# Kernel tuning notes

Hardware: AMD Instinct MI355X
Metric: run time of the kernel (lower is better)

Reference implementation:

```python
import jax, jax.numpy as jnp
import numpy as np

# ---- static config (matches init_kwargs) ----
B, CIN, COUT, L = 8, 64, 64, 32768
K, STRIDE, PAD, DIL = 5, 1, 2, 1
G, DG = 4, 2                      # groups, deformable_groups_per_groups
GDG = G * DG
CD = CIN // GDG                   # channels per deformable group
DW = 7                            # depthwise kernel size of offset/mask branch
OFFSET_SCALE = 4.0
EPS = 1e-5
LOUT = (L + 2 * PAD - DIL * (K - 1) - 1) // STRIDE + 1


def setup_inputs() -> dict:
    key = jax.random.key(0)
    ks = jax.random.split(key, 8)
    s = 0.02
    f32 = jnp.float32
    return {
        "x": jax.random.normal(ks[0], (B, CIN, L), f32),
        # offset branch: depthwise conv -> per-channel groupnorm -> 1x1 conv
        "dw_off_w": (jax.random.normal(ks[1], (CIN, 1, DW), f32) * s),
        "dw_off_b": jnp.zeros((CIN,), f32),
        "gn_off_w": jnp.ones((CIN,), f32),
        "gn_off_b": jnp.zeros((CIN,), f32),
        "pw_off_w": (jax.random.normal(ks[2], (GDG * K, CIN), f32) * s),
        "pw_off_b": jnp.zeros((GDG * K,), f32),
        # attn-mask branch (same structure); final bias init to ones per repo
        "dw_m_w": (jax.random.normal(ks[3], (CIN, 1, DW), f32) * s),
        "dw_m_b": jnp.zeros((CIN,), f32),
        "gn_m_w": jnp.ones((CIN,), f32),
        "gn_m_b": jnp.zeros((CIN,), f32),
        "pw_m_w": (jax.random.normal(ks[4], (GDG * K, CIN), f32) * s),
        "pw_m_b": jnp.ones((GDG * K,), f32),
        # main conv weight (Cout, Cin/G, K) and bias, normal(0, 0.02)
        "weight": (jax.random.normal(ks[5], (COUT, CIN // G, K), f32) * s),
        "bias": (jax.random.normal(ks[6], (COUT,), f32) * s),
    }


def _dwconv(x, w, b):
    # depthwise conv1d, padding (DW-1)//2, groups = CIN
    y = jax.lax.conv_general_dilated(
        x, w, window_strides=(1,), padding=[((DW - 1) // 2, (DW - 1) // 2)],
        feature_group_count=CIN, dimension_numbers=("NCH", "OIH", "NCH"))
    return y + b[None, :, None]


def _gn_per_channel(x, g, b):
    # GroupNorm with num_groups == num_channels: normalize each channel over L
    mu = jnp.mean(x, axis=-1, keepdims=True)
    var = jnp.var(x, axis=-1, keepdims=True)
    return (x - mu) * jax.lax.rsqrt(var + EPS) * g[None, :, None] + b[None, :, None]


def _branch(x, dw_w, dw_b, gn_g, gn_b, pw_w, pw_b):
    h = _gn_per_channel(_dwconv(x, dw_w, dw_b), gn_g, gn_b)
    return jnp.einsum("oc,bcl->bol", pw_w, h) + pw_b[None, :, None]


def _deform_conv1d(x, offset, attn, weight, bias):
    # x: (B,CIN,L); offset/attn: (B,GDG*K,LOUT)
    xg = x.reshape(B, G, DG, CD, L)
    off = offset.reshape(B, G, DG, K, LOUT)
    # base sampling grid: l*stride - pad + k*dil   -> (K, LOUT)
    base = (jnp.arange(LOUT) * STRIDE - PAD)[None, :] + (jnp.arange(K) * DIL)[:, None]
    p = base.astype(x.dtype)[None, None, None] + off          # (B,G,DG,K,LOUT)
    p0 = jnp.floor(p)
    w1 = p - p0                                               # linear-interp weight
    p0i = p0.astype(jnp.int32)

    def gather(idx):
        valid = ((idx >= 0) & (idx < L)).astype(x.dtype)
        idxc = jnp.clip(idx, 0, L - 1).reshape(B, G, DG, 1, K * LOUT)
        idxc = jnp.broadcast_to(idxc, (B, G, DG, CD, K * LOUT))
        v = jnp.take_along_axis(xg, idxc, axis=-1).reshape(B, G, DG, CD, K, LOUT)
        return v * valid[:, :, :, None]

    sampled = gather(p0i) * (1.0 - w1)[:, :, :, None] + gather(p0i + 1) * w1[:, :, :, None]
    sampled = sampled * attn.reshape(B, G, DG, 1, K, LOUT)
    wg = weight.reshape(G, COUT // G, DG, CD, K)
    out = jnp.einsum("godck,bgdckl->bgol", wg, sampled).reshape(B, COUT, LOUT)
    return out + bias[None, :, None]


def reference(x, dw_off_w, dw_off_b, gn_off_w, gn_off_b, pw_off_w, pw_off_b,
              dw_m_w, dw_m_b, gn_m_w, gn_m_b, pw_m_w, pw_m_b, weight, bias):
    offset = _branch(x, dw_off_w, dw_off_b, gn_off_w, gn_off_b, pw_off_w, pw_off_b) * OFFSET_SCALE
    attn = _branch(x, dw_m_w, dw_m_b, gn_m_w, gn_m_b, pw_m_w, pw_m_b)
    # softmax modulation over the K kernel taps within each deformable group
    attn = jax.nn.softmax(attn.reshape(B, GDG, K, LOUT), axis=2).reshape(B, GDG * K, LOUT)
    return _deform_conv1d(x, offset, attn, weight, bias)
```

## Files before the change

### kernel.cpp

```cpp
#include <hip/hip_runtime.h>
#include <hip/hip_bf16.h>
#include <hip/hip_fp16.h>

typedef unsigned int   uint;
typedef unsigned short ushort;

#define NB   8
#define NC   64
#define LL   32768
#define KK   5
#define NG   4
#define NDG  2
#define NGD  8
#define NCD  8
#define NOFF 40
#define DWK  7
#define XROW (LL + 16)

typedef _Float16 f16x8 __attribute__((ext_vector_type(8)));
typedef float    f32x4 __attribute__((ext_vector_type(4)));

__device__ __forceinline__ uint pkrtz(float a, float b) {
  typedef __fp16 fp16x2n __attribute__((ext_vector_type(2)));
  fp16x2n h = __builtin_amdgcn_cvt_pkrtz(a, b);
  union { fp16x2n h; uint u; } v; v.h = h; return v.u;
}

__global__ __launch_bounds__(256) void k_prep(
    const float* __restrict__ pwA, const float* __restrict__ pwM,
    const float* __restrict__ mw,
    float* __restrict__ wtA, float* __restrict__ wtM, ushort* __restrict__ Wf)
{
  int idx = blockIdx.x * 256 + threadIdx.x;
  if (idx < 2560) {
    int c = idx / 40, o = idx % 40;
    wtA[idx] = pwA[o * NC + c];
  } else if (idx < 5120) {
    int j = idx - 2560;
    int c = j / 40, o = j % 40;
    wtM[j] = pwM[o * NC + c];
  } else if (idx < 11264) {
    int j  = idx - 5120;
    int jj = j & 7;
    int l  = (j >> 3) & 63;
    int gt = j >> 9;
    int t  = gt % 3, g = gt / 3;
    int o  = l & 15;
    int kq = t * 32 + ((l >> 4) << 3) + jj;
    float val = 0.f;
    if (kq < 80) {
      int ktap = kq >> 3, c = kq & 7;
      int d = ktap / 5, kh = ktap % 5;
      val = mw[((g * 16 + o) * 16 + d * 8 + c) * KK + kh];
    }
    Wf[j] = __half_as_ushort(__float2half(val));
  }
}

__device__ __forceinline__ void load8f(float* dst, const float* __restrict__ row,
                                       int start)
{
  if (start >= 0 && start + 8 <= LL) {
    float4 a = *(const float4*)(row + start);
    float4 b = *(const float4*)(row + start + 4);
    dst[0] = a.x; dst[1] = a.y; dst[2] = a.z; dst[3] = a.w;
    dst[4] = b.x; dst[5] = b.y; dst[6] = b.z; dst[7] = b.w;
  } else {
#pragma unroll
    for (int j = 0; j < 8; ++j) {
      int p = start + j;
      dst[j] = (p >= 0 && p < LL) ? row[p] : 0.f;
    }
  }
}

__global__ __launch_bounds__(256) void k_stat(
    const float* __restrict__ x,
    const float* __restrict__ dwAw, const float* __restrict__ dwAb,
    const float* __restrict__ dwMw, const float* __restrict__ dwMb,
    ushort* __restrict__ xT, float4* __restrict__ partial)
{
  __shared__ __align__(16) ushort lx[8 * 256];
  int tid  = threadIdx.x;
  int lblk = blockIdx.x & 127;
  int gd   = (blockIdx.x >> 7) & 7;
  int b    = blockIdx.x >> 10;
  int c    = tid >> 5;
  int q    = tid & 31;
  int l0   = lblk << 8;
  int lb   = l0 + q * 8;
  int ch   = gd * 8 + c;
  const float* row = x + (size_t)(b * NC + ch) * LL;

  float v[24];
  load8f(v + 0,  row, lb - 8);
  load8f(v + 8,  row, lb);
  load8f(v + 16, row, lb + 8);

  {
    uint4 xr;
    xr.x = pkrtz(v[8],  v[9]);
    xr.y = pkrtz(v[10], v[11]);
    xr.z = pkrtz(v[12], v[13]);
    xr.w = pkrtz(v[14], v[15]);
    *(uint4*)(lx + c * 256 + q * 8) = xr;
  }

  float wa[DWK], wm[DWK];
#pragma unroll
  for (int j = 0; j < DWK; ++j) {
    wa[j] = dwAw[ch * DWK + j];
    wm[j] = dwMw[ch * DWK + j];
  }
  float ba = dwAb[ch], bm = dwMb[ch];

  float sa = 0.f, qa = 0.f, sm = 0.f, qm = 0.f;
#pragma unroll
  for (int u = 0; u < 8; ++u) {
    float ya = ba, ym = bm;
#pragma unroll
    for (int j = 0; j < DWK; ++j) {
      float xv = v[5 + u + j];
      ya += wa[j] * xv;
      ym += wm[j] * xv;
    }
    sa += ya; qa += ya * ya;
    sm += ym; qm += ym * ym;
  }

#pragma unroll
  for (int m = 1; m < 32; m <<= 1) {
    sa += __shfl_xor(sa, m);
    qa += __shfl_xor(qa, m);
    sm += __shfl_xor(sm, m);
    qm += __shfl_xor(qm, m);
  }
  if (q == 0)
    partial[((size_t)(b * NC + ch) << 7) + lblk] = make_float4(sa, qa, sm, qm);

  __syncthreads();
  {
    uint4 pk;
    pk.x = (uint)lx[0 * 256 + tid] | ((uint)lx[1 * 256 + tid] << 16);
    pk.y = (uint)lx[2 * 256 + tid] | ((uint)lx[3 * 256 + tid] << 16);
    pk.z = (uint)lx[4 * 256 + tid] | ((uint)lx[5 * 256 + tid] << 16);
    pk.w = (uint)lx[6 * 256 + tid] | ((uint)lx[7 * 256 + tid] << 16);
    size_t rowbase = (size_t)(b * NGD + gd) * (size_t)XROW;
    *(uint4*)(xT + (rowbase + 8 + (size_t)(l0 + tid)) * 8) = pk;
    if (tid < 8) {
      uint4 z = {0, 0, 0, 0};
      if (lblk == 0)   *(uint4*)(xT + (rowbase + tid) * 8) = z;
      if (lblk == 127) *(uint4*)(xT + (rowbase + 8 + LL + tid) * 8) = z;
    }
  }
}

__global__ __launch_bounds__(256) void k_fin(
    const float4* __restrict__ partial,
    const float* __restrict__ gnAw, const float* __restrict__ gnAb,
    const float* __restrict__ gnMw, const float* __restrict__ gnMb,
    const float* __restrict__ wtA, const float* __restrict__ wtM,
    const float* __restrict__ pbA, const float* __restrict__ pbM,
    ushort* __restrict__ wFp, float* __restrict__ biasPt)
{
  __shared__ float4 pr[256];
  __shared__ float gA[64], cA[64], gM[64], cM[64];
  __shared__ float sbA[40], sbM[40];
  int b = blockIdx.x;
  int t = threadIdx.x;
  {
    int c = t & 63, seg = t >> 6;
    const float4* pp = partial + ((size_t)(b * NC + c) << 7);
    float4 s = make_float4(0.f, 0.f, 0.f, 0.f);
    for (int i = seg; i < 128; i += 4) {
      float4 u = pp[i];
      s.x += u.x; s.y += u.y; s.z += u.z; s.w += u.w;
    }
    pr[t] = s;
  }
  __syncthreads();
  if (t < 64) {
    float4 a0 = pr[t], a1 = pr[t + 64], a2 = pr[t + 128], a3 = pr[t + 192];
    float sx = a0.x + a1.x + a2.x + a3.x;
    float sy = a0.y + a1.y + a2.y + a3.y;
    float sz = a0.z + a1.z + a2.z + a3.z;
    float sw = a0.w + a1.w + a2.w + a3.w;
    float mua = sx / LL, vara = sy / LL - mua * mua;
    float mum = sz / LL, varm = sw / LL - mum * mum;
    float ga = gnAw[t] * rsqrtf(vara + 1e-5f);
    float gm = gnMw[t] * rsqrtf(varm + 1e-5f);
    gA[t] = ga; cA[t] = gnAb[t] - mua * ga;
    gM[t] = gm; cM[t] = gnMb[t] - mum * gm;
  }
  __syncthreads();
  if (t < 40) {
    float sA = 0.f, sM = 0.f;
    for (int c = 0; c < 64; ++c) {
      sA += wtA[c * 40 + t] * cA[c];
      sM += wtM[c * 40 + t] * cM[c];
    }
    sbA[t] = 4.f * (pbA[t] + sA);
    sbM[t] = pbM[t] + sM;
  }
  for (int idx = t; idx < 8192; idx += 256) {
    int br = idx >> 12;
    int e  = idx & 4095;
    int g  = e >> 10;
    int ks = (e >> 9) & 1;
    int ln = (e >> 3) & 63;
    int j  = e & 7;
    int rr = ln & 15;
    int c  = ks * 32 + ((ln >> 4) << 3) + j;
    float v = 0.f;
    if (rr < 10) {
      int o = 10 * g + rr;
      v = br ? wtM[c * 40 + o] * gM[c] : 4.f * wtA[c * 40 + o] * gA[c];
    }
    wFp[(size_t)b * 8192 + idx] = __half_as_ushort(__float2half(v));
  }
  __syncthreads();
  if (t < 128) {
    int br = t >> 6, g = (t >> 4) & 3, m = t & 15;
    float v = 0.f;
    if (m < 10) v = br ? sbM[10 * g + m] : sbA[10 * g + m];
    biasPt[b * 128 + t] = v;
  }
}

__global__ __launch_bounds__(256) void k_pd(
    const float* __restrict__ x,
    const float* __restrict__ dwAw, const float* __restrict__ dwAb,
    const float* __restrict__ dwMw, const float* __restrict__ dwMb,
    const ushort* __restrict__ xT,
    const ushort* __restrict__ wFp, const float* __restrict__ biasPt,
    const ushort* __restrict__ Wf, const float* __restrict__ bias,
    float* __restrict__ out)
{
  __shared__ __align__(16) char S[4 * 12288];
  int tid = threadIdx.x;
  int w   = tid >> 6;
  int ln  = tid & 63;
  int h   = ln >> 4;
  int col = ln & 15;
  int b   = blockIdx.x >> 9;
  int lb0 = (blockIdx.x & 511) << 6;

  {
    int cc = tid >> 2;
    int q  = tid & 3;
    int p0 = lb0 + q * 16;
    const float* row = x + (size_t)(b * NC + cc) * LL;
    float v[32];
    load8f(v + 0,  row, p0 - 8);
    load8f(v + 8,  row, p0);
    load8f(v + 16, row, p0 + 8);
    load8f(v + 24, row, p0 + 16);
    float wa[DWK], wm[DWK];
#pragma unroll
    for (int j = 0; j < DWK; ++j) {
      wa[j] = dwAw[cc * DWK + j];
      wm[j] = dwMw[cc * DWK + j];
    }
    float ba = dwAb[cc], bm = dwMb[cc];
    uint wbuf[16];
#pragma unroll
    for (int u = 0; u < 16; ++u) {
      float ya = ba, ym = bm;
#pragma unroll
      for (int j = 0; j < DWK; ++j) {
        float xv = v[5 + u + j];
        ya += wa[j] * xv;
        ym += wm[j] * xv;
      }
      wbuf[u] = pkrtz(ya, ym);
    }
    int hc = (cc >> 3) & 3;
    char* base = S + cc * 256;
    int xr = (hc << 6) ^ ((cc & 3) << 4);
#pragma unroll
    for (int i = 0; i < 4; ++i) {
      uint4 wv;
      wv.x = wbuf[i * 4 + 0]; wv.y = wbuf[i * 4 + 1];
      wv.z = wbuf[i * 4 + 2]; wv.w = wbuf[i * 4 + 3];
      *(uint4*)(base + ((q * 64 + i * 16) ^ xr)) = wv;
    }
  }

  const uint4* wFb = (const uint4*)(wFp + (size_t)b * 8192);
  f16x8 afA[2], afM[2];
#pragma unroll
  for (int ks = 0; ks < 2; ++ks) {
    union { uint4 u; f16x8 v; } cvA, cvM;
    cvA.u = wFb[(w * 2 + ks) * 64 + ln];
    cvM.u = wFb[512 + (w * 2 + ks) * 64 + ln];
    afA[ks] = cvA.v; afM[ks] = cvM.v;
  }
  f32x4 accA[4], accM[4];
  {
    float4 bvA = *(const float4*)(biasPt + b * 128 + w * 16 + h * 4);
    float4 bvM = *(const float4*)(biasPt + b * 128 + 64 + w * 16 + h * 4);
#pragma unroll
    for (int nt = 0; nt < 4; ++nt) {
      accA[nt][0]=bvA.x; accA[nt][1]=bvA.y; accA[nt][2]=bvA.z; accA[nt][3]=bvA.w;
      accM[nt][0]=bvM.x; accM[nt][1]=bvM.y; accM[nt][2]=bvM.z; accM[nt][3]=bvM.w;
    }
  }
  __syncthreads();

  __builtin_amdgcn_s_setprio(1);
#pragma unroll
  for (int nt = 0; nt < 4; ++nt) {
#pragma unroll
    for (int ks = 0; ks < 2; ++ks) {
      const char* rowb = S + (ks * 32 + h * 8) * 256;
      int p4 = (((nt * 16 + col) << 2)) ^ (h << 6);
      uint r0 = *(const uint*)(rowb + 0 * 256 + (p4 ^ 0));
      uint r1 = *(const uint*)(rowb + 1 * 256 + (p4 ^ 16));
      uint r2 = *(const uint*)(rowb + 2 * 256 + (p4 ^ 32));
      uint r3 = *(const uint*)(rowb + 3 * 256 + (p4 ^ 48));
      uint r4 = *(const uint*)(rowb + 4 * 256 + (p4 ^ 0));
      uint r5 = *(const uint*)(rowb + 5 * 256 + (p4 ^ 16));
      uint r6 = *(const uint*)(rowb + 6 * 256 + (p4 ^ 32));
      uint r7 = *(const uint*)(rowb + 7 * 256 + (p4 ^ 48));
      union { uint u[4]; f16x8 v; } bA, bM;
      bA.u[0] = __builtin_amdgcn_perm(r1, r0, 0x05040100u);
      bA.u[1] = __builtin_amdgcn_perm(r3, r2, 0x05040100u);
      bA.u[2] = __builtin_amdgcn_perm(r5, r4, 0x05040100u);
      bA.u[3] = __builtin_amdgcn_perm(r7, r6, 0x05040100u);
      bM.u[0] = __builtin_amdgcn_perm(r1, r0, 0x07060302u);
      bM.u[1] = __builtin_amdgcn_perm(r3, r2, 0x07060302u);
      bM.u[2] = __builtin_amdgcn_perm(r5, r4, 0x07060302u);
      bM.u[3] = __builtin_amdgcn_perm(r7, r6, 0x07060302u);
      accA[nt] = __builtin_amdgcn_mfma_f32_16x16x32_f16(afA[ks], bA.v,
                                                        accA[nt], 0, 0, 0);
      accM[nt] = __builtin_amdgcn_mfma_f32_16x16x32_f16(afM[ks], bM.v,
                                                        accM[nt], 0, 0, 0);
    }
  }
  __builtin_amdgcn_s_setprio(0);
  __syncthreads();

  char* wb = S + w * 12288;
#pragma unroll
  for (int r = 0; r < 4; ++r) {
    int s = h * 4 + r;
    if (s < 10) {
#pragma unroll
      for (int nt = 0; nt < 4; ++nt) {
        int pos = nt * 16 + col;
        *(float*)(wb + (s << 8) + (pos << 2)) = accA[nt][r];
        *(float*)(wb + 2560 + (s << 8) + (pos << 2)) = accM[nt][r];
      }
    }
  }
  float off[10], lg[10];
#pragma unroll
  for (int s = 0; s < 10; ++s) {
    off[s] = *(const float*)(wb + (s << 8) + (ln << 2));
    lg[s]  = *(const float*)(wb + 2560 + (s << 8) + (ln << 2));
  }
  float at[10];
  {
    float m0 = fmaxf(fmaxf(fmaxf(lg[0], lg[1]), fmaxf(lg[2], lg[3])), lg[4]);
    float m1 = fmaxf(fmaxf(fmaxf(lg[5], lg[6]), fmaxf(lg[7], lg[8])), lg[9]);
    float e[10], s0 = 0.f, s1 = 0.f;
#pragma unroll
    for (int j = 0; j < 5; ++j) { e[j] = __expf(lg[j] - m0); s0 += e[j]; }
#pragma unroll
    for (int j = 5; j < 10; ++j) { e[j] = __expf(lg[j] - m1); s1 += e[j]; }
    float r0 = 1.f / s0, r1 = 1.f / s1;
#pragma unroll
    for (int j = 0; j < 5; ++j)  at[j] = e[j] * r0;
#pragma unroll
    for (int j = 5; j < 10; ++j) at[j] = e[j] * r1;
  }

  int g = w;
  int l = lb0 + ln;

  f16x8 af[3];
#pragma unroll
  for (int t = 0; t < 3; ++t) {
    union { uint4 u; f16x8 hh; } cv;
    cv.u = ((const uint4*)Wf)[(g * 3 + t) * 64 + ln];
    af[t] = cv.hh;
  }
  int orow = (ln >> 4) << 2;
  float4 b4 = *(const float4*)(bias + g * 16 + orow);
  f32x4 acc[4];
#pragma unroll
  for (int nb = 0; nb < 4; ++nb) {
    acc[nb][0] = b4.x; acc[nb][1] = b4.y; acc[nb][2] = b4.z; acc[nb][3] = b4.w;
  }

  char* sb  = wb;
  int nbase = ln * 192;
  int msk   = (ln & 7) << 4;

  {
    f16x8 Z = {};
    *(f16x8*)(sb + ((nbase + 160) ^ msk)) = Z;
    *(f16x8*)(sb + ((nbase + 176) ^ msk)) = Z;
  }

#pragma unroll
  for (int d = 0; d < NDG; ++d) {
    const ushort* xr = xT + (size_t)(b * NGD + g * 2 + d) * (size_t)XROW * 8;
#pragma unroll
    for (int kh = 0; kh < KK; ++kh) {
      int s = d * KK + kh;
      float p = (float)(l - 2 + kh) + off[s];
      p = fminf(fmaxf(p, -1.f), 32768.f);
      float p0f = floorf(p);
      float w1  = p - p0f;
      int   i0  = (int)p0f;
      float f0 = (1.f - w1) * at[s];
      float f1 = w1 * at[s];
      _Float16 a0 = (_Float16)f0;
      _Float16 a1 = (_Float16)f1;
      f16x8 F0 = {a0, a0, a0, a0, a0, a0, a0, a0};
      f16x8 F1 = {a1, a1, a1, a1, a1, a1, a1, a1};
      const ushort* qp = xr + (size_t)(i0 + 8) * 8;
      f16x8 X0 = *(const f16x8*)qp;
      f16x8 X1 = *(const f16x8*)(qp + 8);
      f16x8 S8 = X0 * F0 + X1 * F1;
      *(f16x8*)(sb + ((nbase + s * 16) ^ msk)) = S8;
    }
  }

  int rb0 = (ln & 15) * 192 + ((ln >> 4) << 4);
  __builtin_amdgcn_s_setprio(1);
#pragma unroll
  for (int nb = 0; nb < 4; ++nb) {
#pragma unroll
    for (int t = 0; t < 3; ++t) {
      f16x8 bf = *(const f16x8*)(sb + ((rb0 + nb * 3072 + t * 64) ^ msk));
      acc[nb] = __builtin_amdgcn_mfma_f32_16x16x32_f16(af[t], bf, acc[nb],
                                                       0, 0, 0);
    }
  }
  __builtin_amdgcn_s_setprio(0);

  float* ob = out + (size_t)(b * NC + g * 16 + orow) * LL + lb0 + (ln & 15);
#pragma unroll
  for (int nb = 0; nb < 4; ++nb) {
#pragma unroll
    for (int r = 0; r < 4; ++r)
      ob[(size_t)r * LL + (nb << 4)] = acc[nb][r];
  }
}

extern "C" void kernel_launch(void* const* d_in, const int* in_sizes, int n_in,
                              void* d_out, int out_size, void* d_ws, size_t ws_size,
                              hipStream_t stream)
{
  const float* x    = (const float*)d_in[0];
  const float* dwAw = (const float*)d_in[1];
  const float* dwAb = (const float*)d_in[2];
  const float* gnAw = (const float*)d_in[3];
  const float* gnAb = (const float*)d_in[4];
  const float* pwAw = (const float*)d_in[5];
  const float* pwAb = (const float*)d_in[6];
  const float* dwMw = (const float*)d_in[7];
  const float* dwMb = (const float*)d_in[8];
  const float* gnMw = (const float*)d_in[9];
  const float* gnMb = (const float*)d_in[10];
  const float* pwMw = (const float*)d_in[11];
  const float* pwMb = (const float*)d_in[12];
  const float* mw   = (const float*)d_in[13];
  const float* bias = (const float*)d_in[14];
  float* out = (float*)d_out;

  float* wtA = (float*)d_ws;
  float* wtM = wtA + 2560;
  ushort* Wf = (ushort*)(wtM + 2560);
  ushort* wFp = Wf + 6144;
  float* biasPt = (float*)(wFp + 65536);
  float4* partial = (float4*)(biasPt + 1024);
  ushort* xT = (ushort*)(partial + 65536);

  hipLaunchKernelGGL(k_prep, dim3(44), dim3(256), 0, stream,
                     pwAw, pwMw, mw, wtA, wtM, Wf);
  hipLaunchKernelGGL(k_stat, dim3(NB * NGD * 128), dim3(256), 0, stream,
                     x, dwAw, dwAb, dwMw, dwMb, xT, partial);
  hipLaunchKernelGGL(k_fin, dim3(NB), dim3(256), 0, stream,
                     partial, gnAw, gnAb, gnMw, gnMb, wtA, wtM, pwAb, pwMb,
                     wFp, biasPt);
  hipLaunchKernelGGL(k_pd, dim3(NB * 512), dim3(256), 0, stream,
                     x, dwAw, dwAb, dwMw, dwMb, xT, wFp, biasPt, Wf, bias, out);
}
```

Baseline: 202.5 us.

## Stream deformable samples through a small per-wave LDS buffer per k-step

Instead of writing all 10 bilinear-sampled tap vectors per lane into a 12KB per-wave swizzled LDS staging area and then running all MFMAs, the kernel now builds one 4-tap slice (one MFMA k-step) at a time in a 5KB per-wave buffer with an 80-byte row stride, then immediately issues the 4 MFMAs for that slice. This cuts shared memory per block from 48KB to 20KB to allow more resident blocks and interleaves gather with MFMA work. It drops the XOR swizzle, which may add LDS bank conflicts, and reuses the buffer across k-steps without explicit barriers, relying on in-wave ordering.

New measurement: 199.5 us. About the same (-1.5%).

```diff
diff --git a/kernel.cpp b/kernel.cpp
--- a/kernel.cpp
+++ b/kernel.cpp
@@ -236,7 +236,7 @@
     const ushort* __restrict__ Wf, const float* __restrict__ bias,
     float* __restrict__ out)
 {
-  __shared__ __align__(16) char S[4 * 12288];
+  __shared__ __align__(16) char S[20480];
   int tid = threadIdx.x;
   int w   = tid >> 6;
   int ln  = tid & 63;
@@ -340,7 +340,7 @@
   __builtin_amdgcn_s_setprio(0);
   __syncthreads();
 
-  char* wb = S + w * 12288;
+  char* wb = S + w * 5120;
 #pragma unroll
   for (int r = 0; r < 4; ++r) {
     int s = h * 4 + r;
@@ -393,53 +393,48 @@
     acc[nb][0] = b4.x; acc[nb][1] = b4.y; acc[nb][2] = b4.z; acc[nb][3] = b4.w;
   }
 
-  char* sb  = wb;
-  int nbase = ln * 192;
-  int msk   = (ln & 7) << 4;
-
-  {
-    f16x8 Z = {};
-    *(f16x8*)(sb + ((nbase + 160) ^ msk)) = Z;
-    *(f16x8*)(sb + ((nbase + 176) ^ msk)) = Z;
-  }
-
-#pragma unroll
-  for (int d = 0; d < NDG; ++d) {
-    const ushort* xr = xT + (size_t)(b * NGD + g * 2 + d) * (size_t)XROW * 8;
-#pragma unroll
-    for (int kh = 0; kh < KK; ++kh) {
-      int s = d * KK + kh;
-      float p = (float)(l - 2 + kh) + off[s];
-      p = fminf(fmaxf(p, -1.f), 32768.f);
-      float p0f = floorf(p);
-      float w1  = p - p0f;
-      int   i0  = (int)p0f;
-      float f0 = (1.f - w1) * at[s];
-      float f1 = w1 * at[s];
-      _Float16 a0 = (_Float16)f0;
-      _Float16 a1 = (_Float16)f1;
-      f16x8 F0 = {a0, a0, a0, a0, a0, a0, a0, a0};
-      f16x8 F1 = {a1, a1, a1, a1, a1, a1, a1, a1};
-      const ushort* qp = xr + (size_t)(i0 + 8) * 8;
-      f16x8 X0 = *(const f16x8*)qp;
-      f16x8 X1 = *(const f16x8*)(qp + 8);
-      f16x8 S8 = X0 * F0 + X1 * F1;
-      *(f16x8*)(sb + ((nbase + s * 16) ^ msk)) = S8;
-    }
-  }
-
-  int rb0 = (ln & 15) * 192 + ((ln >> 4) << 4);
-  __builtin_amdgcn_s_setprio(1);
-#pragma unroll
-  for (int nb = 0; nb < 4; ++nb) {
-#pragma unroll
-    for (int t = 0; t < 3; ++t) {
-      f16x8 bf = *(const f16x8*)(sb + ((rb0 + nb * 3072 + t * 64) ^ msk));
+  char* buf = wb;
+  int rbase = ((ln & 15)) * 80 + ((ln >> 4) << 4);
+#pragma unroll
+  for (int t = 0; t < 3; ++t) {
+#pragma unroll
+    for (int sl = 0; sl < 4; ++sl) {
+      int s = 4 * t + sl;
+      char* dst = buf + ln * 80 + sl * 16;
+      if (s < 10) {
+        const ushort* xr = xT + (size_t)(b * NGD + g * 2 + (s >= KK ? 1 : 0))
+                                * (size_t)XROW * 8;
+        int kh = s >= KK ? s - KK : s;
+        float p = (float)(l - 2 + kh) + off[s];
+        p = fminf(fmaxf(p, -1.f), 32768.f);
+        float p0f = floorf(p);
+        float w1  = p - p0f;
+        int   i0  = (int)p0f;
+        float f0 = (1.f - w1) * at[s];
+        float f1 = w1 * at[s];
+        _Float16 a0 = (_Float16)f0;
+        _Float16 a1 = (_Float16)f1;
+        f16x8 F0 = {a0, a0, a0, a0, a0, a0, a0, a0};
+        f16x8 F1 = {a1, a1, a1, a1, a1, a1, a1, a1};
+        const ushort* qp = xr + (size_t)(i0 + 8) * 8;
+        f16x8 X0 = *(const f16x8*)qp;
+        f16x8 X1 = *(const f16x8*)(qp + 8);
+        f16x8 S8 = X0 * F0 + X1 * F1;
+        *(f16x8*)dst = S8;
+      } else {
+        f16x8 Z = {};
+        *(f16x8*)dst = Z;
+      }
+    }
+    __builtin_amdgcn_s_setprio(1);
+#pragma unroll
+    for (int nb = 0; nb < 4; ++nb) {
+      f16x8 bf = *(const f16x8*)(buf + nb * 16 * 80 + rbase);
       acc[nb] = __builtin_amdgcn_mfma_f32_16x16x32_f16(af[t], bf, acc[nb],
                                                        0, 0, 0);
     }
-  }
-  __builtin_amdgcn_s_setprio(0);
+    __builtin_amdgcn_s_setprio(0);
+  }
 
   float* ob = out + (size_t)(b * NC + g * 16 + orow) * LL + lb0 + (ln & 15);
 #pragma unroll
```
